# Optimization experiments

Hardware: AMD Instinct MI355X
Metric: run time of the kernel (lower is better)

The kernel has to match this reference:

```python
import jax, jax.numpy as jnp
import numpy as np

INPUT_DIM, HIDDEN_DIM, OUTPUT_DIM = 60, 256, 402


def setup_inputs() -> dict:
    key = jax.random.key(0)
    ks = jax.random.split(key, 7)
    B, T, J, D = 64, 512, 20, 3
    s_ih = 1.0 / np.sqrt(HIDDEN_DIM)
    return {
        "x": jax.random.normal(ks[0], (B, T, J, D), dtype=jnp.float32),
        "W_ih": jax.random.uniform(ks[1], (4 * HIDDEN_DIM, INPUT_DIM), minval=-s_ih, maxval=s_ih, dtype=jnp.float32),
        "W_hh": jax.random.uniform(ks[2], (4 * HIDDEN_DIM, HIDDEN_DIM), minval=-s_ih, maxval=s_ih, dtype=jnp.float32),
        "b_ih": jax.random.uniform(ks[3], (4 * HIDDEN_DIM,), minval=-s_ih, maxval=s_ih, dtype=jnp.float32),
        "b_hh": jax.random.uniform(ks[4], (4 * HIDDEN_DIM,), minval=-s_ih, maxval=s_ih, dtype=jnp.float32),
        "W_fc": jax.random.uniform(ks[5], (OUTPUT_DIM, HIDDEN_DIM), minval=-s_ih, maxval=s_ih, dtype=jnp.float32),
        "b_fc": jax.random.uniform(ks[6], (OUTPUT_DIM,), minval=-s_ih, maxval=s_ih, dtype=jnp.float32),
    }


def _lstm(x, W_ih, W_hh, b_ih, b_hh):
    # x: [B, T, INPUT_DIM] -> hidden states [B, T, H]
    B = x.shape[0]
    H = W_hh.shape[1]
    # Precompute input contribution to all gates for the whole sequence (one big GEMM)
    xg = jnp.einsum('bti,gi->btg', x, W_ih) + b_ih + b_hh  # [B, T, 4H]

    def step(carry, xt):
        h, c = carry
        gates = xt + h @ W_hh.T  # [B, 4H]; pytorch gate order: i, f, g, o
        i, f, g, o = jnp.split(gates, 4, axis=-1)
        i = jax.nn.sigmoid(i)
        f = jax.nn.sigmoid(f)
        g = jnp.tanh(g)
        o = jax.nn.sigmoid(o)
        c = f * c + i * g
        h = o * jnp.tanh(c)
        return (h, c), h

    h0 = jnp.zeros((B, H), dtype=x.dtype)
    (_, _), hs = jax.lax.scan(step, (h0, h0), jnp.swapaxes(xg, 0, 1))  # hs: [T, B, H]
    return jnp.swapaxes(hs, 0, 1)


def reference(x, W_ih, W_hh, b_ih, b_hh, W_fc, b_fc):
    B, T, J, D = x.shape
    xf = x.reshape(B, T, J * D)
    hs = _lstm(xf, W_ih, W_hh, b_ih, b_hh)  # [B, T, H]
    out = jnp.einsum('bth,oh->bto', hs, W_fc) + b_fc  # [B, T, OUTPUT_DIM]
    return out
```

## Files before the change

### kernel.cpp

```cpp
#include <hip/hip_runtime.h>
#include <hip/hip_fp16.h>

typedef _Float16 half2v __attribute__((ext_vector_type(2)));

#define B_ 64
#define T_ 512
#define H_ 256
#define G4_ 1024
#define IN_ 60
#define O_ 402

#define NREGQ 50
#define NLDSQ 14

__device__ __forceinline__ float fdot2(unsigned int a, unsigned int b, float c) {
  return __builtin_amdgcn_fdot2(__builtin_bit_cast(half2v, a),
                                __builtin_bit_cast(half2v, b), c, false);
}

__device__ __forceinline__ unsigned int pack_h2(float a, float b) {
  unsigned short ua = __half_as_ushort(__float2half(a));
  unsigned short ub = __half_as_ushort(__float2half(b));
  return (unsigned int)ua | ((unsigned int)ub << 16);
}

__device__ __forceinline__ float sigmoid_f(float x) {
  return __fdividef(1.0f, 1.0f + __expf(-x));
}
__device__ __forceinline__ float tanh_f(float x) {
  float ax = fminf(fabsf(x) * 2.0f, 40.0f);
  float e = __expf(ax);
  float r = __fdividef(e - 1.0f, e + 1.0f);
  return copysignf(r, x);
}

__global__ __launch_bounds__(256) void k0_pack(
    const float* __restrict__ wih, const float* __restrict__ whh,
    const float* __restrict__ bih, const float* __restrict__ bhh,
    const float* __restrict__ wfc,
    float* __restrict__ wpih, float* __restrict__ biasp,
    unsigned int* __restrict__ wreg_ws, unsigned int* __restrict__ wlds_ws,
    unsigned int* __restrict__ wfcp) {
  int idx = blockIdx.x * 256 + threadIdx.x;
  if (idx < 61440) {
    int k = idx / 1024, rp = idx % 1024;
    int orig = (rp & 3) * 256 + (rp >> 2);
    wpih[idx] = wih[orig * IN_ + k];
  } else if (idx < 62464) {
    int rp = idx - 61440;
    int orig = (rp & 3) * 256 + (rp >> 2);
    biasp[rp] = bih[orig] + bhh[orig];
  } else if (idx < 193536) {
    int i2 = idx - 62464;
    int l = i2 >> 8;
    int i = i2 & 255;
    int jq = i >> 2, p = i & 3;
    int cc = jq >> 2, q = jq & 3;
    int u = l >> 1, hf = l & 1;
    int P = hf * 64 + cc * 4 + p;
    int row = q * 256 + u;
    unsigned int pk = pack_h2(whh[row * 256 + 2 * P], whh[row * 256 + 2 * P + 1]);
    if (jq < NREGQ) wreg_ws[(jq * 512 + l) * 4 + p] = pk;
    else            wlds_ws[((jq - NREGQ) * 512 + l) * 4 + p] = pk;
  } else if (idx < 244992) {
    int i3 = idx - 193536;
    int o = i3 >> 7, P = i3 & 127;
    wfcp[o * 128 + P] = pack_h2(wfc[o * 256 + 2 * P], wfc[o * 256 + 2 * P + 1]);
  }
}

template <bool F32>
__global__ __launch_bounds__(256, 2) void k1_xgemm(
    const float* __restrict__ x, const float* __restrict__ wpih,
    const float* __restrict__ biasp, void* __restrict__ xg_v) {
  __shared__ float xt[IN_ * 64];
  const int l = threadIdx.x, blk = blockIdx.x;
  for (int i = l; i < IN_ * 64; i += 256) {
    int k = i >> 6, bt = i & 63;
    xt[i] = x[(size_t)(blk * 64 + bt) * IN_ + k];
  }
  __syncthreads();
  float4 bias4 = *(const float4*)&biasp[4 * l];
  float* xg_f = (float*)xg_v;
  unsigned int* xg_h = (unsigned int*)xg_v;
  for (int half = 0; half < 2; ++half) {
    float4 a[32];
#pragma unroll
    for (int j = 0; j < 32; ++j) a[j] = bias4;
    for (int k = 0; k < IN_; ++k) {
      float4 w4 = *(const float4*)&wpih[k * G4_ + 4 * l];
#pragma unroll
      for (int j4 = 0; j4 < 8; ++j4) {
        float4 xv = *(const float4*)&xt[k * 64 + half * 32 + j4 * 4];
        float xs[4] = {xv.x, xv.y, xv.z, xv.w};
#pragma unroll
        for (int jj = 0; jj < 4; ++jj) {
          float xc = xs[jj];
          float4& A = a[j4 * 4 + jj];
          A.x = fmaf(w4.x, xc, A.x); A.y = fmaf(w4.y, xc, A.y);
          A.z = fmaf(w4.z, xc, A.z); A.w = fmaf(w4.w, xc, A.w);
        }
      }
    }
#pragma unroll
    for (int j = 0; j < 32; ++j) {
      size_t bt = (size_t)blk * 64 + half * 32 + j;
      if constexpr (F32) {
        *(float4*)&xg_f[bt * G4_ + 4 * l] = a[j];
      } else {
        uint2 pk;
        pk.x = pack_h2(a[j].x, a[j].y);
        pk.y = pack_h2(a[j].z, a[j].w);
        *(uint2*)&xg_h[bt * (G4_ / 2) + 2 * l] = pk;
      }
    }
  }
}

template <bool F32>
__global__ __launch_bounds__(512, 2) void k2_lstm(
    const void* __restrict__ xg_v, const uint4* __restrict__ wreg_ws,
    const uint4* __restrict__ wlds_ws, unsigned short* __restrict__ hs) {
  __shared__ uint4 wlds[NLDSQ * 512];
  __shared__ unsigned int hq4[2][2][68];
  const int l = threadIdx.x;
  const int b = blockIdx.x;
  const int hf = l & 1;
  for (int i = l; i < NLDSQ * 512; i += 512) wlds[i] = wlds_ws[i];
  if (l < 64)        hq4[0][0][l] = 0u;
  else if (l < 128)  hq4[0][1][l - 64] = 0u;

  uint4 wr[NREGQ];
#pragma unroll
  for (int j = 0; j < NREGQ; ++j) {
    wr[j] = wreg_ws[j * 512 + l];
    asm("" : "+v"(wr[j].x));
    asm("" : "+v"(wr[j].y));
    asm("" : "+v"(wr[j].z));
    asm("" : "+v"(wr[j].w));
  }

  const unsigned int* xgu = (const unsigned int*)xg_v;
  const float2* xgf2 = (const float2*)xg_v;
  float2 xf2; unsigned int xh;
  if constexpr (F32) xf2 = xgf2[(size_t)b * T_ * 512 + l];
  else               xh  = xgu[(size_t)b * T_ * 512 + l];
  float c = 0.0f;
  __syncthreads();
  for (int t = 0; t < T_; ++t) {
    float lo, hi;
    if constexpr (F32) { lo = xf2.x; hi = xf2.y; }
    else {
      half2v p = __builtin_bit_cast(half2v, xh);
      lo = (float)p[0]; hi = (float)p[1];
    }
    float a0 = hf ? 0.0f : lo, a1 = hf ? 0.0f : hi;
    float a2 = hf ? lo : 0.0f, a3 = hf ? hi : 0.0f;
    int tn = (t < T_ - 1) ? (t + 1) : t;
    if constexpr (F32) xf2 = xgf2[(size_t)(b * T_ + tn) * 512 + l];
    else               xh  = xgu[(size_t)(b * T_ + tn) * 512 + l];

    const uint4* hB = (const uint4*)hq4[t & 1][hf];
#pragma unroll
    for (int cc = 0; cc < 16; ++cc) {
      uint4 hq = hB[cc];
      unsigned int wv[16];
#pragma unroll
      for (int q = 0; q < 4; ++q) {
        int jq = cc * 4 + q;
        if (jq < NREGQ) {
          wv[q*4+0] = wr[jq].x; wv[q*4+1] = wr[jq].y;
          wv[q*4+2] = wr[jq].z; wv[q*4+3] = wr[jq].w;
        } else {
          uint4 v = wlds[(jq - NREGQ) * 512 + l];
          wv[q*4+0] = v.x; wv[q*4+1] = v.y; wv[q*4+2] = v.z; wv[q*4+3] = v.w;
        }
      }
      a0 = fdot2(wv[ 0], hq.x, a0); a0 = fdot2(wv[ 1], hq.y, a0);
      a0 = fdot2(wv[ 2], hq.z, a0); a0 = fdot2(wv[ 3], hq.w, a0);
      a1 = fdot2(wv[ 4], hq.x, a1); a1 = fdot2(wv[ 5], hq.y, a1);
      a1 = fdot2(wv[ 6], hq.z, a1); a1 = fdot2(wv[ 7], hq.w, a1);
      a2 = fdot2(wv[ 8], hq.x, a2); a2 = fdot2(wv[ 9], hq.y, a2);
      a2 = fdot2(wv[10], hq.z, a2); a2 = fdot2(wv[11], hq.w, a2);
      a3 = fdot2(wv[12], hq.x, a3); a3 = fdot2(wv[13], hq.y, a3);
      a3 = fdot2(wv[14], hq.z, a3); a3 = fdot2(wv[15], hq.w, a3);
    }
    a0 += __shfl_xor(a0, 1); a1 += __shfl_xor(a1, 1);
    a2 += __shfl_xor(a2, 1); a3 += __shfl_xor(a3, 1);
    float ig = sigmoid_f(a0), fg = sigmoid_f(a1);
    float gg = tanh_f(a2),    og = sigmoid_f(a3);
    c = fg * c + ig * gg;
    float h = og * tanh_f(c);
    unsigned int hbits = (unsigned int)__half_as_ushort(__float2half(h));
    unsigned int hnext = (unsigned int)__shfl_xor((int)hbits, 2);
    if ((l & 3) == 0) {
      unsigned int pk = hbits | (hnext << 16);
      int d = l >> 2;
      hq4[(t & 1) ^ 1][d >> 6][d & 63] = pk;
      ((unsigned int*)hs)[(size_t)(b * T_ + t) * 128 + d] = pk;
    }
    __syncthreads();
  }
}

__global__ __launch_bounds__(256, 2) void k3_out(
    const unsigned short* __restrict__ hs, const unsigned int* __restrict__ wfcp,
    const float* __restrict__ bfc, float* __restrict__ out) {
  __shared__ unsigned int ht[64 * 128];
  const int l = threadIdx.x, blk = blockIdx.x;
  const unsigned int* hsrc = (const unsigned int*)hs + (size_t)blk * 64 * 128;
  for (int i = l; i < 64 * 128; i += 256) ht[i] = hsrc[i];
  __syncthreads();
  const int c1 = l;
  const int c2 = 256 + l;
  const bool has2 = (c2 < O_);
  const int c2r = has2 ? c2 : 0;
  float b1 = bfc[c1], b2 = bfc[c2r];
  for (int btc = 0; btc < 4; ++btc) {
    float a1[16], a2[16];
#pragma unroll
    for (int j = 0; j < 16; ++j) { a1[j] = b1; a2[j] = b2; }
    for (int Pc = 0; Pc < 8; ++Pc) {
      uint4 wq1[4], wq2[4];
#pragma unroll
      for (int p4 = 0; p4 < 4; ++p4) {
        wq1[p4] = *(const uint4*)&wfcp[c1 * 128 + Pc * 16 + 4 * p4];
        wq2[p4] = *(const uint4*)&wfcp[c2r * 128 + Pc * 16 + 4 * p4];
      }
#pragma unroll
      for (int j = 0; j < 16; ++j) {
        const unsigned int* hr = &ht[(btc * 16 + j) * 128 + Pc * 16];
#pragma unroll
        for (int p4 = 0; p4 < 4; ++p4) {
          uint4 hv = *(const uint4*)&hr[4 * p4];
          a1[j] = fdot2(wq1[p4].x, hv.x, a1[j]);
          a1[j] = fdot2(wq1[p4].y, hv.y, a1[j]);
          a1[j] = fdot2(wq1[p4].z, hv.z, a1[j]);
          a1[j] = fdot2(wq1[p4].w, hv.w, a1[j]);
          a2[j] = fdot2(wq2[p4].x, hv.x, a2[j]);
          a2[j] = fdot2(wq2[p4].y, hv.y, a2[j]);
          a2[j] = fdot2(wq2[p4].z, hv.z, a2[j]);
          a2[j] = fdot2(wq2[p4].w, hv.w, a2[j]);
        }
      }
    }
#pragma unroll
    for (int j = 0; j < 16; ++j) {
      size_t bt = (size_t)blk * 64 + btc * 16 + j;
      out[bt * O_ + c1] = a1[j];
      if (has2) out[bt * O_ + c2] = a2[j];
    }
  }
}

extern "C" void kernel_launch(void* const* d_in, const int* in_sizes, int n_in,
                              void* d_out, int out_size, void* d_ws, size_t ws_size,
                              hipStream_t stream) {
  const float* x   = (const float*)d_in[0];
  const float* wih = (const float*)d_in[1];
  const float* whh = (const float*)d_in[2];
  const float* bih = (const float*)d_in[3];
  const float* bhh = (const float*)d_in[4];
  const float* wfc = (const float*)d_in[5];
  const float* bfc = (const float*)d_in[6];
  float* out = (float*)d_out;
  char* ws = (char*)d_ws;

  const size_t HS_BYTES = (size_t)B_ * T_ * H_ * 2;
  const size_t XG_F32   = (size_t)B_ * T_ * G4_ * 4;
  const size_t WREG_B   = (size_t)NREGQ * 512 * 16;
  const size_t WLDS_B   = (size_t)NLDSQ * 512 * 16;
  const size_t WPIH_B   = (size_t)IN_ * G4_ * 4;
  const size_t BIAS_B   = (size_t)G4_ * 4;
  const size_t WFCP_B   = (size_t)O_ * 128 * 4;
  const size_t TAIL = HS_BYTES + WREG_B + WLDS_B + WPIH_B + BIAS_B + WFCP_B;

  bool f32xg = (ws_size >= XG_F32 + TAIL);
  size_t xg_bytes = f32xg ? XG_F32 : ((size_t)B_ * T_ * G4_ * 2);

  char* xg    = ws;
  char* hsb   = ws + xg_bytes;
  char* wregp = hsb + HS_BYTES;
  char* wldsp = wregp + WREG_B;
  char* wpihp = wldsp + WLDS_B;
  char* biasp = wpihp + WPIH_B;
  char* wfcpp = biasp + BIAS_B;

  hipLaunchKernelGGL(k0_pack, dim3(957), dim3(256), 0, stream,
                     wih, whh, bih, bhh, wfc,
                     (float*)wpihp, (float*)biasp,
                     (unsigned int*)wregp, (unsigned int*)wldsp,
                     (unsigned int*)wfcpp);
  if (f32xg) {
    hipLaunchKernelGGL((k1_xgemm<true>), dim3(512), dim3(256), 0, stream,
                       x, (const float*)wpihp, (const float*)biasp, (void*)xg);
    hipLaunchKernelGGL((k2_lstm<true>), dim3(64), dim3(512), 0, stream,
                       (const void*)xg, (const uint4*)wregp, (const uint4*)wldsp,
                       (unsigned short*)hsb);
  } else {
    hipLaunchKernelGGL((k1_xgemm<false>), dim3(512), dim3(256), 0, stream,
                       x, (const float*)wpihp, (const float*)biasp, (void*)xg);
    hipLaunchKernelGGL((k2_lstm<false>), dim3(64), dim3(512), 0, stream,
                       (const void*)xg, (const uint4*)wregp, (const uint4*)wldsp,
                       (unsigned short*)hsb);
  }
  hipLaunchKernelGGL(k3_out, dim3(512), dim3(256), 0, stream,
                     (const unsigned short*)hsb, (const unsigned int*)wfcpp,
                     bfc, out);
}
```

Baseline: 982.2 us.

## Split recurrent weights across VGPRs, LDS and global streaming with interleaved placement

Recurrent W_hh quads are now spread over three tiers: 28 in registers, 19 in LDS and 17 re-read from global memory (L2/cache) on every timestep. The placement follows the gate quad index, so each cc chunk mixes register, LDS and global sources and the latencies can overlap. This frees registers that may help occupancy or avoid spills, but it adds per-step global loads of about 140KB per block onto the serial recurrence.

```diff
diff --git a/kernel.cpp b/kernel.cpp
--- a/kernel.cpp
+++ b/kernel.cpp
@@ -10,8 +10,30 @@
 #define IN_ 60
 #define O_ 402
 
-#define NREGQ 50
-#define NLDSQ 14
+#define NREGQ 28
+#define NLDSQ 19
+#define NSTRQ 17
+
+__host__ __device__ __forceinline__ constexpr bool is_vgpr_q(int jq) {
+  int cc = jq >> 2, q = jq & 3;
+  return (q == 0) || (q == 1 && cc >= 4);
+}
+__host__ __device__ __forceinline__ constexpr int vg_slot(int jq) {
+  int cc = jq >> 2, q = jq & 3;
+  return (q == 0) ? cc : 16 + (cc - 4);
+}
+__host__ __device__ __forceinline__ constexpr bool is_lds_q(int jq) {
+  int cc = jq >> 2, q = jq & 3;
+  return (q == 3) || (q == 2 && cc >= 13);
+}
+__host__ __device__ __forceinline__ constexpr int lds_slot(int jq) {
+  int cc = jq >> 2, q = jq & 3;
+  return (q == 3) ? cc : 16 + (cc - 13);
+}
+__host__ __device__ __forceinline__ constexpr int str_slot(int jq) {
+  int cc = jq >> 2, q = jq & 3;
+  return (q == 1) ? cc : 4 + cc;
+}
 
 __device__ __forceinline__ float fdot2(unsigned int a, unsigned int b, float c) {
   return __builtin_amdgcn_fdot2(__builtin_bit_cast(half2v, a),
@@ -40,7 +62,7 @@
     const float* __restrict__ wfc,
     float* __restrict__ wpih, float* __restrict__ biasp,
     unsigned int* __restrict__ wreg_ws, unsigned int* __restrict__ wlds_ws,
-    unsigned int* __restrict__ wfcp) {
+    unsigned int* __restrict__ wstr_ws, unsigned int* __restrict__ wfcp) {
   int idx = blockIdx.x * 256 + threadIdx.x;
   if (idx < 61440) {
     int k = idx / 1024, rp = idx % 1024;
@@ -60,8 +82,9 @@
     int P = hf * 64 + cc * 4 + p;
     int row = q * 256 + u;
     unsigned int pk = pack_h2(whh[row * 256 + 2 * P], whh[row * 256 + 2 * P + 1]);
-    if (jq < NREGQ) wreg_ws[(jq * 512 + l) * 4 + p] = pk;
-    else            wlds_ws[((jq - NREGQ) * 512 + l) * 4 + p] = pk;
+    if (is_vgpr_q(jq))     wreg_ws[(vg_slot(jq) * 512 + l) * 4 + p] = pk;
+    else if (is_lds_q(jq)) wlds_ws[(lds_slot(jq) * 512 + l) * 4 + p] = pk;
+    else                   wstr_ws[(str_slot(jq) * 512 + l) * 4 + p] = pk;
   } else if (idx < 244992) {
     int i3 = idx - 193536;
     int o = i3 >> 7, P = i3 & 127;
@@ -120,7 +143,8 @@
 template <bool F32>
 __global__ __launch_bounds__(512, 2) void k2_lstm(
     const void* __restrict__ xg_v, const uint4* __restrict__ wreg_ws,
-    const uint4* __restrict__ wlds_ws, unsigned short* __restrict__ hs) {
+    const uint4* __restrict__ wlds_ws, const uint4* __restrict__ wstr_ws,
+    unsigned short* __restrict__ hs) {
   __shared__ uint4 wlds[NLDSQ * 512];
   __shared__ unsigned int hq4[2][2][68];
   const int l = threadIdx.x;
@@ -164,26 +188,17 @@
 #pragma unroll
     for (int cc = 0; cc < 16; ++cc) {
       uint4 hq = hB[cc];
-      unsigned int wv[16];
 #pragma unroll
       for (int q = 0; q < 4; ++q) {
-        int jq = cc * 4 + q;
-        if (jq < NREGQ) {
-          wv[q*4+0] = wr[jq].x; wv[q*4+1] = wr[jq].y;
-          wv[q*4+2] = wr[jq].z; wv[q*4+3] = wr[jq].w;
-        } else {
-          uint4 v = wlds[(jq - NREGQ) * 512 + l];
-          wv[q*4+0] = v.x; wv[q*4+1] = v.y; wv[q*4+2] = v.z; wv[q*4+3] = v.w;
-        }
-      }
-      a0 = fdot2(wv[ 0], hq.x, a0); a0 = fdot2(wv[ 1], hq.y, a0);
-      a0 = fdot2(wv[ 2], hq.z, a0); a0 = fdot2(wv[ 3], hq.w, a0);
-      a1 = fdot2(wv[ 4], hq.x, a1); a1 = fdot2(wv[ 5], hq.y, a1);
-      a1 = fdot2(wv[ 6], hq.z, a1); a1 = fdot2(wv[ 7], hq.w, a1);
-      a2 = fdot2(wv[ 8], hq.x, a2); a2 = fdot2(wv[ 9], hq.y, a2);
-      a2 = fdot2(wv[10], hq.z, a2); a2 = fdot2(wv[11], hq.w, a2);
-      a3 = fdot2(wv[12], hq.x, a3); a3 = fdot2(wv[13], hq.y, a3);
-      a3 = fdot2(wv[14], hq.z, a3); a3 = fdot2(wv[15], hq.w, a3);
+        const int jq = cc * 4 + q;
+        uint4 w;
+        if (is_vgpr_q(jq))     w = wr[vg_slot(jq)];
+        else if (is_lds_q(jq)) w = wlds[lds_slot(jq) * 512 + l];
+        else                   w = wstr_ws[str_slot(jq) * 512 + l];
+        float& aq = (q == 0) ? a0 : (q == 1) ? a1 : (q == 2) ? a2 : a3;
+        aq = fdot2(w.x, hq.x, aq); aq = fdot2(w.y, hq.y, aq);
+        aq = fdot2(w.z, hq.z, aq); aq = fdot2(w.w, hq.w, aq);
+      }
     }
     a0 += __shfl_xor(a0, 1); a1 += __shfl_xor(a1, 1);
     a2 += __shfl_xor(a2, 1); a3 += __shfl_xor(a3, 1);
@@ -270,10 +285,11 @@
   const size_t XG_F32   = (size_t)B_ * T_ * G4_ * 4;
   const size_t WREG_B   = (size_t)NREGQ * 512 * 16;
   const size_t WLDS_B   = (size_t)NLDSQ * 512 * 16;
+  const size_t WSTR_B   = (size_t)NSTRQ * 512 * 16;
   const size_t WPIH_B   = (size_t)IN_ * G4_ * 4;
   const size_t BIAS_B   = (size_t)G4_ * 4;
   const size_t WFCP_B   = (size_t)O_ * 128 * 4;
-  const size_t TAIL = HS_BYTES + WREG_B + WLDS_B + WPIH_B + BIAS_B + WFCP_B;
+  const size_t TAIL = HS_BYTES + WREG_B + WLDS_B + WSTR_B + WPIH_B + BIAS_B + WFCP_B;
 
   bool f32xg = (ws_size >= XG_F32 + TAIL);
   size_t xg_bytes = f32xg ? XG_F32 : ((size_t)B_ * T_ * G4_ * 2);
@@ -282,7 +298,8 @@
   char* hsb   = ws + xg_bytes;
   char* wregp = hsb + HS_BYTES;
   char* wldsp = wregp + WREG_B;
-  char* wpihp = wldsp + WLDS_B;
+  char* wstrp = wldsp + WLDS_B;
+  char* wpihp = wstrp + WSTR_B;
   char* biasp = wpihp + WPIH_B;
   char* wfcpp = biasp + BIAS_B;
 
@@ -290,19 +307,19 @@
                      wih, whh, bih, bhh, wfc,
                      (float*)wpihp, (float*)biasp,
                      (unsigned int*)wregp, (unsigned int*)wldsp,
-                     (unsigned int*)wfcpp);
+                     (unsigned int*)wstrp, (unsigned int*)wfcpp);
   if (f32xg) {
     hipLaunchKernelGGL((k1_xgemm<true>), dim3(512), dim3(256), 0, stream,
                        x, (const float*)wpihp, (const float*)biasp, (void*)xg);
     hipLaunchKernelGGL((k2_lstm<true>), dim3(64), dim3(512), 0, stream,
                        (const void*)xg, (const uint4*)wregp, (const uint4*)wldsp,
-                       (unsigned short*)hsb);
+                       (const uint4*)wstrp, (unsigned short*)hsb);
   } else {
     hipLaunchKernelGGL((k1_xgemm<false>), dim3(512), dim3(256), 0, stream,
                        x, (const float*)wpihp, (const float*)biasp, (void*)xg);
     hipLaunchKernelGGL((k2_lstm<false>), dim3(64), dim3(512), 0, stream,
                        (const void*)xg, (const uint4*)wregp, (const uint4*)wldsp,
-                       (unsigned short*)hsb);
+                       (const uint4*)wstrp, (unsigned short*)hsb);
   }
   hipLaunchKernelGGL(k3_out, dim3(512), dim3(256), 0, stream,
                      (const unsigned short*)hsb, (const unsigned int*)wfcpp,
```

Measured after the change: 964.3 us, median of 2. Within noise of the previous version (-1.8%).
